# Kernel optimization log

Hardware: AMD Instinct MI355X
Metric: run time of the kernel (lower is better)

The kernel has to match this reference:

```python
import jax, jax.numpy as jnp
import numpy as np

N = 50000          # nodes
E = 800000         # edges (avg degree 16)
IN = 128           # input feature dim
HID = 64           # hidden dim per head
HEADS = 2          # attention heads (all but last layer)
OUT = 64           # out_dim (last layer, 1 head)
NC = 2             # num_classes
NEG_SLOPE = 0.2    # dgl GATConv leaky_relu slope


def setup_inputs() -> dict:
    key = jax.random.key(0)
    ks = jax.random.split(key, 20)
    rn = lambda k, shape, s=0.05: (jax.random.normal(k, shape, jnp.float32) * s)
    W_IO = HID * HEADS  # 128, width between GAT layers
    return {
        "x": rn(ks[0], (N, IN), 1.0),
        "src": jax.random.randint(ks[1], (E,), 0, N, dtype=jnp.int32),
        "dst": jax.random.randint(ks[2], (E,), 0, N, dtype=jnp.int32),
        # embedding_h: Linear(IN, HID*HEADS)
        "W_emb": rn(ks[3], (IN, W_IO)),
        "b_emb": jnp.zeros((W_IO,), jnp.float32),
        # GAT layer 0: in 128 -> 2 heads x 64
        "W0": rn(ks[4], (W_IO, HEADS * HID)),
        "al0": rn(ks[5], (HEADS, HID)),
        "ar0": rn(ks[6], (HEADS, HID)),
        "b0": jnp.zeros((HEADS * HID,), jnp.float32),
        # GAT layer 1: in 128 -> 2 heads x 64
        "W1": rn(ks[7], (W_IO, HEADS * HID)),
        "al1": rn(ks[8], (HEADS, HID)),
        "ar1": rn(ks[9], (HEADS, HID)),
        "b1": jnp.zeros((HEADS * HID,), jnp.float32),
        # GAT layer 2 (last): in 128 -> 1 head x OUT
        "W2": rn(ks[10], (W_IO, 1 * OUT)),
        "al2": rn(ks[11], (1, OUT)),
        "ar2": rn(ks[12], (1, OUT)),
        "b2": jnp.zeros((OUT,), jnp.float32),
        # edge scorer: Linear(2*OUT, NC)
        "Ws": rn(ks[13], (2 * OUT, NC)),
        "bs": jnp.zeros((NC,), jnp.float32),
    }


def gat_layer(h, src, dst, W, al, ar, b):
    """dgl GATConv + elu (GATLayer with batch_norm=False, residual=False)."""
    heads, out = al.shape
    feat = (h @ W).reshape(-1, heads, out)            # [N,H,D]
    el = jnp.sum(feat * al, axis=-1)                  # [N,H]
    er = jnp.sum(feat * ar, axis=-1)                  # [N,H]
    e = jax.nn.leaky_relu(el[src] + er[dst], NEG_SLOPE)  # [E,H]
    # edge softmax over incoming edges of each dst node
    emax = jax.ops.segment_max(e, dst, num_segments=N)   # [N,H]
    ex = jnp.exp(e - emax[dst])                          # [E,H]
    denom = jax.ops.segment_sum(ex, dst, num_segments=N) # [N,H]
    alpha = ex / jnp.where(denom[dst] > 0, denom[dst], 1.0)
    msg = feat[src] * alpha[:, :, None]                  # [E,H,D]
    rst = jax.ops.segment_sum(msg, dst, num_segments=N)  # [N,H,D]
    rst = rst.reshape(-1, heads * out) + b
    return jax.nn.elu(rst)


def reference(x, W_emb, b_emb, W0, al0, ar0, b0, W1, al1, ar1, b1,
              W2, al2, ar2, b2, Ws, bs, src, dst):
    h = x @ W_emb + b_emb                    # embedding_h (dropout p -> eval/identity)
    h = gat_layer(h, src, dst, W0, al0, ar0, b0)
    h = gat_layer(h, src, dst, W1, al1, ar1, b1)
    h = gat_layer(h, src, dst, W2, al2, ar2, b2)   # [N, OUT]
    # edge scorer on the scored subgraph: concat(src_h, dst_h) -> Linear
    he = jnp.concatenate([h[src], h[dst]], axis=1)  # [E, 2*OUT]
    return he @ Ws + bs                             # [E, NC]
```

## Files before the change

### kernel.cpp

```cpp
#include <hip/hip_runtime.h>
#include <hip/hip_bf16.h>
#include <math.h>


constexpr float SLOPE = 0.2f;

typedef __attribute__((ext_vector_type(8))) short bf16x8;
typedef __attribute__((ext_vector_type(4))) float f32x4;

__device__ __forceinline__ float b2f(unsigned short u) {
  union { unsigned int i; float f; } v;
  v.i = ((unsigned int)u) << 16;
  return v.f;
}
__device__ __forceinline__ unsigned short f2b(float f) {
  unsigned int x = __float_as_uint(f);
  unsigned int r = (x + 0x7fffu + ((x >> 16) & 1u)) >> 16;
  return (unsigned short)r;
}

__global__ void prep_wt_all(const float* __restrict__ Wa,
                            const float* __restrict__ Wb,
                            const float* __restrict__ Wc,
                            const float* __restrict__ Wd,
                            unsigned short* __restrict__ Ta,
                            unsigned short* __restrict__ Tb,
                            unsigned short* __restrict__ Tc,
                            unsigned short* __restrict__ Td) {
  int i = blockIdx.x * 256 + threadIdx.x;
  const float* W; unsigned short* T; int M; int off;
  if (i < 16384)      { W = Wa; T = Ta; M = 128; off = i; }
  else if (i < 32768) { W = Wb; T = Tb; M = 128; off = i - 16384; }
  else if (i < 49152) { W = Wc; T = Tc; M = 128; off = i - 32768; }
  else if (i < 57344) { W = Wd; T = Td; M = 64;  off = i - 49152; }
  else return;
  int k = off / M, m = off - k * M;
  T[m * 128 + k] = f2b(W[off]);
}

template<int M, bool AF32>
__global__ __launch_bounds__(256)
void gemm_mfma(const void* __restrict__ Xv,
               const unsigned short* __restrict__ Wt,
               const float* __restrict__ bias,
               const float* __restrict__ al, const float* __restrict__ ar,
               unsigned short* __restrict__ Yb,
               float* __restrict__ el, float* __restrict__ er, int N) {
  constexpr int NT = M / 16;
  constexpr int H = M / 64;

  const int tid = threadIdx.x;
  const int wave = tid >> 6;
  const int lane = tid & 63;
  const int r = lane & 15;
  const int kg = lane >> 4;
  const int rowbase = blockIdx.x * 64 + wave * 16;
  int grow = rowbase + r;
  int growc = grow < N ? grow : N - 1;

  f32x4 acc[NT];
  #pragma unroll
  for (int t = 0; t < NT; ++t) acc[t] = (f32x4){0.f, 0.f, 0.f, 0.f};

  #pragma unroll
  for (int kk = 0; kk < 4; ++kk) {
    const int k0 = kk * 32 + kg * 8;
    bf16x8 a;
    if constexpr (AF32) {
      const float* X = (const float*)Xv;
      const float4* xp =
          reinterpret_cast<const float4*>(X + (size_t)growc * 128 + k0);
      float4 x0 = xp[0], x1 = xp[1];
      a[0] = (short)f2b(x0.x); a[1] = (short)f2b(x0.y);
      a[2] = (short)f2b(x0.z); a[3] = (short)f2b(x0.w);
      a[4] = (short)f2b(x1.x); a[5] = (short)f2b(x1.y);
      a[6] = (short)f2b(x1.z); a[7] = (short)f2b(x1.w);
    } else {
      const unsigned short* Xb = (const unsigned short*)Xv;
      a = *reinterpret_cast<const bf16x8*>(Xb + (size_t)growc * 128 + k0);
    }
    #pragma unroll
    for (int t = 0; t < NT; ++t) {
      bf16x8 b = *reinterpret_cast<const bf16x8*>(
          Wt + (size_t)(t * 16 + r) * 128 + k0);
      acc[t] = __builtin_amdgcn_mfma_f32_16x16x32_bf16(a, b, acc[t], 0, 0, 0);
    }
  }

  float bv[NT];
  #pragma unroll
  for (int t = 0; t < NT; ++t) bv[t] = bias ? bias[t * 16 + r] : 0.f;
  float alv[NT], arv[NT];
  if (al != nullptr) {
    #pragma unroll
    for (int t = 0; t < NT; ++t) {
      alv[t] = al[t * 16 + r];
      arv[t] = ar[t * 16 + r];
    }
  }

  #pragma unroll
  for (int j = 0; j < 4; ++j) {
    int orow = rowbase + kg * 4 + j;
    bool ok = orow < N;
    if (ok) {
      #pragma unroll
      for (int t = 0; t < NT; ++t)
        Yb[(size_t)orow * M + t * 16 + r] = f2b(acc[t][j] + bv[t]);
    }
    if (al != nullptr) {
      float pl0 = 0.f, pr0 = 0.f, pl1 = 0.f, pr1 = 0.f;
      #pragma unroll
      for (int t = 0; t < 4; ++t) {
        pl0 += acc[t][j] * alv[t];
        pr0 += acc[t][j] * arv[t];
      }
      if constexpr (H == 2) {
        #pragma unroll
        for (int t = 4; t < 8; ++t) {
          pl1 += acc[t][j] * alv[t];
          pr1 += acc[t][j] * arv[t];
        }
      }
      #pragma unroll
      for (int off = 1; off < 16; off <<= 1) {
        pl0 += __shfl_xor(pl0, off);
        pr0 += __shfl_xor(pr0, off);
        if constexpr (H == 2) {
          pl1 += __shfl_xor(pl1, off);
          pr1 += __shfl_xor(pr1, off);
        }
      }
      if (r == 0 && ok) {
        if constexpr (H == 2) {
          el[orow * 2 + 0] = pl0; el[orow * 2 + 1] = pl1;
          er[orow * 2 + 0] = pr0; er[orow * 2 + 1] = pr1;
        } else {
          el[orow] = pl0;
          er[orow] = pr0;
        }
      }
    }
  }
}

__global__ __launch_bounds__(256)
void count_dst(const int* __restrict__ dst, int* __restrict__ cnt, int E) {
  int cls = blockIdx.x & 7;
  int grp = blockIdx.x >> 3;
  int nGrp = gridDim.x >> 3;
  for (int base = grp * 256; base < E; base += nGrp * 256) {
    int i = base + threadIdx.x;
    if (i < E) {
      int d = dst[i];
      if (((d >> 4) & 7) == cls) atomicAdd(&cnt[d], 1);
    }
  }
}

__global__ void scan1(const int* __restrict__ cnt, int* __restrict__ outv,
                      int* __restrict__ bsum, int n) {
  __shared__ int sm[256];
  int tid = threadIdx.x;
  int base = blockIdx.x * 1024 + tid * 4;
  int pre[4];
  int s = 0;
  #pragma unroll
  for (int j = 0; j < 4; ++j) {
    int idx = base + j;
    int v = (idx < n) ? ((cnt[idx] + 7) & ~7) : 0;
    pre[j] = s;
    s += v;
  }
  sm[tid] = s;
  __syncthreads();
  for (int off = 1; off < 256; off <<= 1) {
    int a = (tid >= off) ? sm[tid - off] : 0;
    __syncthreads();
    sm[tid] += a;
    __syncthreads();
  }
  int excl = sm[tid] - s;
  #pragma unroll
  for (int j = 0; j < 4; ++j) {
    int idx = base + j;
    if (idx < n) outv[idx] = excl + pre[j];
  }
  if (tid == 255) bsum[blockIdx.x] = sm[255];
}

__global__ void scan2(const int* __restrict__ bsum, int* __restrict__ btop,
                      int nb, int* __restrict__ row_last) {
  if (threadIdx.x == 0 && blockIdx.x == 0) {
    int s = 0;
    for (int i = 0; i < nb; ++i) { btop[i] = s; s += bsum[i]; }
    *row_last = s;
  }
}

__global__ void scan3(int* __restrict__ rp, int* __restrict__ cur,
                      const int* __restrict__ btop, int n) {
  int i = blockIdx.x * blockDim.x + threadIdx.x;
  if (i < n) {
    int v = rp[i] + btop[i >> 10];
    rp[i] = v;
    cur[i] = v;
  }
}

__global__ __launch_bounds__(256)
void scatter_edges(const int* __restrict__ src, const int* __restrict__ dst,
                   int* __restrict__ cur, int* __restrict__ s_csr, int E) {
  int cls = blockIdx.x & 7;
  int grp = blockIdx.x >> 3;
  int nGrp = gridDim.x >> 3;
  for (int base = grp * 256; base < E; base += nGrp * 256) {
    int i = base + threadIdx.x;
    if (i < E) {
      int d = dst[i];
      if (((d >> 4) & 7) == cls) {
        int p = atomicAdd(&cur[d], 1);
        s_csr[p] = src[i];
      }
    }
  }
}

template<int H>
__global__ __launch_bounds__(256)
void edge_prep(const int* __restrict__ s_csr, const float* __restrict__ el,
               const float* __restrict__ er, const int* __restrict__ rp,
               const int* __restrict__ ends, float2* __restrict__ edat,
               int N, int EP) {
  int tid = threadIdx.x;
  int node = blockIdx.x * 16 + (tid >> 4);
  int sl = tid & 15;
  if (node >= N) return;
  int beg = rp[node];
  int rend = ends[node];
  int pend = rp[node + 1];
  if constexpr (H == 2) {
    float2 re = reinterpret_cast<const float2*>(er)[node];
    for (int p = beg + sl; p < rend; p += 16) {
      int s = s_csr[p];
      float2 le = reinterpret_cast<const float2*>(el)[s];
      float e0 = le.x + re.x;
      float e1 = le.y + re.y;
      e0 = e0 > 0.f ? e0 : SLOPE * e0;
      e1 = e1 > 0.f ? e1 : SLOPE * e1;
      float sb = __int_as_float(s);
      edat[p] = make_float2(__expf(e0), sb);
      edat[(size_t)EP + p] = make_float2(__expf(e1), sb);
    }
    int p2 = rend + sl;
    if (p2 < pend) {
      edat[p2] = make_float2(0.f, __int_as_float(0));
      edat[(size_t)EP + p2] = make_float2(0.f, __int_as_float(0));
    }
  } else {
    float re = er[node];
    for (int p = beg + sl; p < rend; p += 16) {
      int s = s_csr[p];
      float ev = el[s] + re;
      ev = ev > 0.f ? ev : SLOPE * ev;
      edat[p] = make_float2(__expf(ev), __int_as_float(s));
    }
    int p2 = rend + sl;
    if (p2 < pend) edat[p2] = make_float2(0.f, __int_as_float(0));
  }
}

template<int H, bool SCORE>
__global__ __launch_bounds__(256)
void gat_aggregate(const unsigned short* __restrict__ featb,
                   const float2* __restrict__ edat,
                   const float* __restrict__ bias,
                   const int* __restrict__ row_ptr,
                   unsigned short* __restrict__ houtb,
                   const float* __restrict__ Wsc,
                   float* __restrict__ ps, float* __restrict__ pd,
                   int N, int EP) {
  int tid = threadIdx.x;
  int pid = blockIdx.x * 16 + (tid >> 4);
  int sl = tid & 15;
  const int NH = N * H;
  bool live = pid < NH;
  int pc = live ? pid : 0;
  int node, head;
  if constexpr (H == 2) { node = pc >> 1; head = pc & 1; }
  else                  { node = pc;      head = 0; }
  int beg = live ? row_ptr[node] : 0;
  int end = live ? row_ptr[node + 1] : 0;

  const int rowoff = head * 64 + sl * 4;
  const float2* edath = edat + (size_t)head * EP;

  float4 acc = make_float4(0.f, 0.f, 0.f, 0.f);
  float den = 0.f;

  for (int p = beg; p < end; p += 8) {
    #pragma unroll
    for (int j = 0; j < 8; ++j) {
      float2 ed = edath[p + j];
      float ex = ed.x;
      int s = __float_as_int(ed.y);
      ushort4 u = *reinterpret_cast<const ushort4*>(
          &featb[(size_t)s * (H * 64) + rowoff]);
      den += ex;
      acc.x += ex * b2f(u.x);
      acc.y += ex * b2f(u.y);
      acc.z += ex * b2f(u.z);
      acc.w += ex * b2f(u.w);
    }
  }

  if (live) {
    float inv = 1.f / (den > 0.f ? den : 1.f);
    float4 bv = reinterpret_cast<const float4*>(bias)[head * 16 + sl];
    float4 r;
    r.x = acc.x * inv + bv.x;
    r.y = acc.y * inv + bv.y;
    r.z = acc.z * inv + bv.z;
    r.w = acc.w * inv + bv.w;
    r.x = r.x > 0.f ? r.x : expm1f(r.x);
    r.y = r.y > 0.f ? r.y : expm1f(r.y);
    r.z = r.z > 0.f ? r.z : expm1f(r.z);
    r.w = r.w > 0.f ? r.w : expm1f(r.w);

    if constexpr (!SCORE) {
      ushort4 o;
      o.x = f2b(r.x); o.y = f2b(r.y); o.z = f2b(r.z); o.w = f2b(r.w);
      *reinterpret_cast<ushort4*>(&houtb[(size_t)pid * 64 + sl * 4]) = o;
    } else {
      float s0 = r.x * Wsc[(4 * sl + 0) * 2] + r.y * Wsc[(4 * sl + 1) * 2] +
                 r.z * Wsc[(4 * sl + 2) * 2] + r.w * Wsc[(4 * sl + 3) * 2];
      float s1 = r.x * Wsc[(4 * sl + 0) * 2 + 1] + r.y * Wsc[(4 * sl + 1) * 2 + 1] +
                 r.z * Wsc[(4 * sl + 2) * 2 + 1] + r.w * Wsc[(4 * sl + 3) * 2 + 1];
      float d0 = r.x * Wsc[(64 + 4 * sl + 0) * 2] + r.y * Wsc[(64 + 4 * sl + 1) * 2] +
                 r.z * Wsc[(64 + 4 * sl + 2) * 2] + r.w * Wsc[(64 + 4 * sl + 3) * 2];
      float d1 = r.x * Wsc[(64 + 4 * sl + 0) * 2 + 1] + r.y * Wsc[(64 + 4 * sl + 1) * 2 + 1] +
                 r.z * Wsc[(64 + 4 * sl + 2) * 2 + 1] + r.w * Wsc[(64 + 4 * sl + 3) * 2 + 1];
      #pragma unroll
      for (int off = 1; off < 16; off <<= 1) {
        s0 += __shfl_xor(s0, off);
        s1 += __shfl_xor(s1, off);
        d0 += __shfl_xor(d0, off);
        d1 += __shfl_xor(d1, off);
      }
      if (sl == 0) {
        ps[node * 2 + 0] = s0;
        ps[node * 2 + 1] = s1;
        pd[node * 2 + 0] = d0;
        pd[node * 2 + 1] = d1;
      }
    }
  }
}

__global__ void score_out(const int* __restrict__ src,
                          const int* __restrict__ dst,
                          const float* __restrict__ ps,
                          const float* __restrict__ pd,
                          const float* __restrict__ bs,
                          float* __restrict__ out, int E) {
  int i = blockIdx.x * blockDim.x + threadIdx.x;
  if (i < E) {
    int s = src[i], d = dst[i];
    float2 a = *reinterpret_cast<const float2*>(ps + (size_t)s * 2);
    float2 b = *reinterpret_cast<const float2*>(pd + (size_t)d * 2);
    float2 o;
    o.x = a.x + b.x + bs[0];
    o.y = a.y + b.y + bs[1];
    *reinterpret_cast<float2*>(out + (size_t)i * 2) = o;
  }
}

extern "C" void kernel_launch(void* const* d_in, const int* in_sizes, int n_in,
                              void* d_out, int out_size, void* d_ws,
                              size_t ws_size, hipStream_t stream) {
  const float* x    = (const float*)d_in[0];
  const int*   src  = (const int*)d_in[1];
  const int*   dst  = (const int*)d_in[2];
  const float* Wemb = (const float*)d_in[3];
  const float* bemb = (const float*)d_in[4];
  const float* W0   = (const float*)d_in[5];
  const float* al0  = (const float*)d_in[6];
  const float* ar0  = (const float*)d_in[7];
  const float* b0   = (const float*)d_in[8];
  const float* W1   = (const float*)d_in[9];
  const float* al1  = (const float*)d_in[10];
  const float* ar1  = (const float*)d_in[11];
  const float* b1   = (const float*)d_in[12];
  const float* W2   = (const float*)d_in[13];
  const float* al2  = (const float*)d_in[14];
  const float* ar2  = (const float*)d_in[15];
  const float* b2   = (const float*)d_in[16];
  const float* Wsc  = (const float*)d_in[17];
  const float* bsc  = (const float*)d_in[18];

  const int N = in_sizes[0] / 128;
  const int E = in_sizes[1];
  float* out = (float*)d_out;
  const int EP = E + 7 * N + 8;

  char* w = (char*)d_ws;
  float2* edat = (float2*)w; w += (size_t)EP * 2 * 8;
  unsigned short* Ab = (unsigned short*)w; w += (size_t)N * 128 * 2;
  unsigned short* Bb = (unsigned short*)w; w += (size_t)N * 128 * 2;
  unsigned short* WembT = (unsigned short*)w; w += 128 * 128 * 2;
  unsigned short* W0T   = (unsigned short*)w; w += 128 * 128 * 2;
  unsigned short* W1T   = (unsigned short*)w; w += 128 * 128 * 2;
  unsigned short* W2T   = (unsigned short*)w; w += 128 * 64 * 2;
  float* el  = (float*)w; w += (size_t)N * 2 * 4;
  float* er  = (float*)w; w += (size_t)N * 2 * 4;
  float* ps  = (float*)w; w += (size_t)N * 2 * 4;
  float* pd  = (float*)w; w += (size_t)N * 2 * 4;
  int* s_csr = (int*)w;   w += (size_t)EP * 4;
  int* cnt   = (int*)w;   w += (size_t)N * 4;
  int* rp    = (int*)w;   w += (size_t)(N + 4) * 4;
  int* cur   = (int*)w;   w += (size_t)N * 4;
  int* bsum  = (int*)w;   w += 4096;
  int* btop  = (int*)w;   w += 4096;

  prep_wt_all<<<(57344 + 255) / 256, 256, 0, stream>>>(
      Wemb, W0, W1, W2, WembT, W0T, W1T, W2T);

  hipMemsetAsync(cnt, 0, (size_t)N * 4, stream);
  count_dst<<<2048, 256, 0, stream>>>(dst, cnt, E);
  int nb = (N + 1023) / 1024;
  scan1<<<nb, 256, 0, stream>>>(cnt, rp, bsum, N);
  scan2<<<1, 64, 0, stream>>>(bsum, btop, nb, rp + N);
  scan3<<<(N + 255) / 256, 256, 0, stream>>>(rp, cur, btop, N);
  scatter_edges<<<2048, 256, 0, stream>>>(src, dst, cur, s_csr, E);

  const int gb = (N + 63) / 64;
  const int nbk = (N + 15) / 16;
  const int pb2 = (N * 2 + 15) / 16;
  const int pb1 = (N * 1 + 15) / 16;

  gemm_mfma<128, true><<<gb, 256, 0, stream>>>(x, WembT, bemb, nullptr,
                                               nullptr, Ab, nullptr, nullptr,
                                               N);

  gemm_mfma<128, false><<<gb, 256, 0, stream>>>(Ab, W0T, nullptr, al0, ar0,
                                                Bb, el, er, N);
  edge_prep<2><<<nbk, 256, 0, stream>>>(s_csr, el, er, rp, cur, edat, N, EP);
  gat_aggregate<2, false><<<pb2, 256, 0, stream>>>(Bb, edat, b0, rp, Ab,
                                                   nullptr, nullptr, nullptr,
                                                   N, EP);
  gemm_mfma<128, false><<<gb, 256, 0, stream>>>(Ab, W1T, nullptr, al1, ar1,
                                                Bb, el, er, N);
  edge_prep<2><<<nbk, 256, 0, stream>>>(s_csr, el, er, rp, cur, edat, N, EP);
  gat_aggregate<2, false><<<pb2, 256, 0, stream>>>(Bb, edat, b1, rp, Ab,
                                                   nullptr, nullptr, nullptr,
                                                   N, EP);
  gemm_mfma<64, false><<<gb, 256, 0, stream>>>(Ab, W2T, nullptr, al2, ar2,
                                               Bb, el, er, N);
  edge_prep<1><<<nbk, 256, 0, stream>>>(s_csr, el, er, rp, cur, edat, N, EP);
  gat_aggregate<1, true><<<pb1, 256, 0, stream>>>(Bb, edat, b2, rp, nullptr,
                                                  Wsc, ps, pd, N, EP);

  score_out<<<(E + 255) / 256, 256, 0, stream>>>(src, dst, ps, pd, bsc, out, E);
}
```

Baseline: 393.3 us.

## Sort nodes into degree bins to balance edge_prep and aggregate work per wave

Computes a per-node degree bucket (padded edge count divided by 8) during the scan, then builds an `order` permutation that groups nodes with equal bucket. edge_prep and gat_aggregate process nodes in that order, so the 16-lane groups sharing a wave walk similar edge counts and less time is lost to divergence. The cost is an extra atomic histogram in scan1, a wave-aggregated atomic placement in scan3, one indirection per node, and a loss of locality in row_ptr, feature writes and output writes, since the permutation scatters node IDs.

Result: slower. 795.1 us (+102.2%).

```diff
diff --git a/kernel.cpp b/kernel.cpp
--- a/kernel.cpp
+++ b/kernel.cpp
@@ -159,7 +159,8 @@
 }
 
 __global__ void scan1(const int* __restrict__ cnt, int* __restrict__ outv,
-                      int* __restrict__ bsum, int n) {
+                      int* __restrict__ bsum, int* __restrict__ binCnt,
+                      int n) {
   __shared__ int sm[256];
   int tid = threadIdx.x;
   int base = blockIdx.x * 1024 + tid * 4;
@@ -168,7 +169,12 @@
   #pragma unroll
   for (int j = 0; j < 4; ++j) {
     int idx = base + j;
-    int v = (idx < n) ? ((cnt[idx] + 7) & ~7) : 0;
+    int c = (idx < n) ? cnt[idx] : 0;
+    int v = (idx < n) ? ((c + 7) & ~7) : 0;
+    if (idx < n) {
+      int t = (c + 7) >> 3; if (t > 63) t = 63;
+      atomicAdd(&binCnt[t], 1);
+    }
     pre[j] = s;
     s += v;
   }
@@ -190,22 +196,52 @@
 }
 
 __global__ void scan2(const int* __restrict__ bsum, int* __restrict__ btop,
-                      int nb, int* __restrict__ row_last) {
+                      int nb, int* __restrict__ row_last,
+                      const int* __restrict__ binCnt,
+                      int* __restrict__ binCur) {
   if (threadIdx.x == 0 && blockIdx.x == 0) {
     int s = 0;
     for (int i = 0; i < nb; ++i) { btop[i] = s; s += bsum[i]; }
     *row_last = s;
+    int s2 = 0;
+    for (int i = 0; i < 64; ++i) { binCur[i] = s2; s2 += binCnt[i]; }
   }
 }
 
 __global__ void scan3(int* __restrict__ rp, int* __restrict__ cur,
-                      const int* __restrict__ btop, int n) {
+                      const int* __restrict__ btop,
+                      const int* __restrict__ cnt, int* __restrict__ binCur,
+                      int* __restrict__ order, int n) {
   int i = blockIdx.x * blockDim.x + threadIdx.x;
-  if (i < n) {
+  int lane = threadIdx.x & 63;
+  bool live = i < n;
+  int t = 0;
+  if (live) {
     int v = rp[i] + btop[i >> 10];
     rp[i] = v;
     cur[i] = v;
-  }
+    int c = cnt[i];
+    t = (c + 7) >> 3; if (t > 63) t = 63;
+  }
+  int pos = 0;
+  bool done = !live;
+  unsigned long long remaining = __ballot(!done);
+  while (remaining) {
+    int srcl = __ffsll((long long)remaining) - 1;
+    int tl = __shfl(t, srcl);
+    unsigned long long same = __ballot(!done && t == tl);
+    if (!done && t == tl) {
+      int lead = __ffsll((long long)same) - 1;
+      int cnt_ = __popcll(same);
+      int basep = 0;
+      if (lane == lead) basep = atomicAdd(&binCur[tl], cnt_);
+      basep = __shfl(basep, lead);
+      pos = basep + __popcll(same & ((1ull << lane) - 1ull));
+      done = true;
+    }
+    remaining &= ~same;
+  }
+  if (live) order[pos] = i;
 }
 
 __global__ __launch_bounds__(256)
@@ -230,12 +266,13 @@
 __global__ __launch_bounds__(256)
 void edge_prep(const int* __restrict__ s_csr, const float* __restrict__ el,
                const float* __restrict__ er, const int* __restrict__ rp,
-               const int* __restrict__ ends, float2* __restrict__ edat,
-               int N, int EP) {
+               const int* __restrict__ ends, const int* __restrict__ order,
+               float2* __restrict__ edat, int N, int EP) {
   int tid = threadIdx.x;
-  int node = blockIdx.x * 16 + (tid >> 4);
+  int g = blockIdx.x * 16 + (tid >> 4);
   int sl = tid & 15;
-  if (node >= N) return;
+  if (g >= N) return;
+  int node = order[g];
   int beg = rp[node];
   int rend = ends[node];
   int pend = rp[node + 1];
@@ -276,6 +313,7 @@
                    const float2* __restrict__ edat,
                    const float* __restrict__ bias,
                    const int* __restrict__ row_ptr,
+                   const int* __restrict__ order,
                    unsigned short* __restrict__ houtb,
                    const float* __restrict__ Wsc,
                    float* __restrict__ ps, float* __restrict__ pd,
@@ -287,8 +325,8 @@
   bool live = pid < NH;
   int pc = live ? pid : 0;
   int node, head;
-  if constexpr (H == 2) { node = pc >> 1; head = pc & 1; }
-  else                  { node = pc;      head = 0; }
+  if constexpr (H == 2) { node = order[pc >> 1]; head = pc & 1; }
+  else                  { node = order[pc];      head = 0; }
   int beg = live ? row_ptr[node] : 0;
   int end = live ? row_ptr[node + 1] : 0;
 
@@ -330,7 +368,8 @@
     if constexpr (!SCORE) {
       ushort4 o;
       o.x = f2b(r.x); o.y = f2b(r.y); o.z = f2b(r.z); o.w = f2b(r.w);
-      *reinterpret_cast<ushort4*>(&houtb[(size_t)pid * 64 + sl * 4]) = o;
+      *reinterpret_cast<ushort4*>(
+          &houtb[((size_t)node * H + head) * 64 + sl * 4]) = o;
     } else {
       float s0 = r.x * Wsc[(4 * sl + 0) * 2] + r.y * Wsc[(4 * sl + 1) * 2] +
                  r.z * Wsc[(4 * sl + 2) * 2] + r.w * Wsc[(4 * sl + 3) * 2];
@@ -417,20 +456,24 @@
   float* pd  = (float*)w; w += (size_t)N * 2 * 4;
   int* s_csr = (int*)w;   w += (size_t)EP * 4;
   int* cnt   = (int*)w;   w += (size_t)N * 4;
+  int* binCnt = (int*)w;  w += 64 * 4;
   int* rp    = (int*)w;   w += (size_t)(N + 4) * 4;
   int* cur   = (int*)w;   w += (size_t)N * 4;
+  int* order = (int*)w;   w += (size_t)N * 4;
+  int* binCur = (int*)w;  w += 64 * 4;
   int* bsum  = (int*)w;   w += 4096;
   int* btop  = (int*)w;   w += 4096;
 
   prep_wt_all<<<(57344 + 255) / 256, 256, 0, stream>>>(
       Wemb, W0, W1, W2, WembT, W0T, W1T, W2T);
 
-  hipMemsetAsync(cnt, 0, (size_t)N * 4, stream);
+  hipMemsetAsync(cnt, 0, (size_t)N * 4 + 64 * 4, stream);
   count_dst<<<2048, 256, 0, stream>>>(dst, cnt, E);
   int nb = (N + 1023) / 1024;
-  scan1<<<nb, 256, 0, stream>>>(cnt, rp, bsum, N);
-  scan2<<<1, 64, 0, stream>>>(bsum, btop, nb, rp + N);
-  scan3<<<(N + 255) / 256, 256, 0, stream>>>(rp, cur, btop, N);
+  scan1<<<nb, 256, 0, stream>>>(cnt, rp, bsum, binCnt, N);
+  scan2<<<1, 64, 0, stream>>>(bsum, btop, nb, rp + N, binCnt, binCur);
+  scan3<<<(N + 255) / 256, 256, 0, stream>>>(rp, cur, btop, cnt, binCur,
+                                             order, N);
   scatter_edges<<<2048, 256, 0, stream>>>(src, dst, cur, s_csr, E);
 
   const int gb = (N + 63) / 64;
@@ -444,21 +487,25 @@
 
   gemm_mfma<128, false><<<gb, 256, 0, stream>>>(Ab, W0T, nullptr, al0, ar0,
                                                 Bb, el, er, N);
-  edge_prep<2><<<nbk, 256, 0, stream>>>(s_csr, el, er, rp, cur, edat, N, EP);
-  gat_aggregate<2, false><<<pb2, 256, 0, stream>>>(Bb, edat, b0, rp, Ab,
-                                                   nullptr, nullptr, nullptr,
-                                                   N, EP);
+  edge_prep<2><<<nbk, 256, 0, stream>>>(s_csr, el, er, rp, cur, order, edat,
+                                        N, EP);
+  gat_aggregate<2, false><<<pb2, 256, 0, stream>>>(Bb, edat, b0, rp, order,
+                                                   Ab, nullptr, nullptr,
+                                                   nullptr, N, EP);
   gemm_mfma<128, false><<<gb, 256, 0, stream>>>(Ab, W1T, nullptr, al1, ar1,
                                                 Bb, el, er, N);
-  edge_prep<2><<<nbk, 256, 0, stream>>>(s_csr, el, er, rp, cur, edat, N, EP);
-  gat_aggregate<2, false><<<pb2, 256, 0, stream>>>(Bb, edat, b1, rp, Ab,
-                                                   nullptr, nullptr, nullptr,
-                                                   N, EP);
+  edge_prep<2><<<nbk, 256, 0, stream>>>(s_csr, el, er, rp, cur, order, edat,
+                                        N, EP);
+  gat_aggregate<2, false><<<pb2, 256, 0, stream>>>(Bb, edat, b1, rp, order,
+                                                   Ab, nullptr, nullptr,
+                                                   nullptr, N, EP);
   gemm_mfma<64, false><<<gb, 256, 0, stream>>>(Ab, W2T, nullptr, al2, ar2,
                                                Bb, el, er, N);
-  edge_prep<1><<<nbk, 256, 0, stream>>>(s_csr, el, er, rp, cur, edat, N, EP);
-  gat_aggregate<1, true><<<pb1, 256, 0, stream>>>(Bb, edat, b2, rp, nullptr,
-                                                  Wsc, ps, pd, N, EP);
+  edge_prep<1><<<nbk, 256, 0, stream>>>(s_csr, el, er, rp, cur, order, edat,
+                                        N, EP);
+  gat_aggregate<1, true><<<pb1, 256, 0, stream>>>(Bb, edat, b2, rp, order,
+                                                  nullptr, Wsc, ps, pd,
+                                                  N, EP);
 
   score_out<<<(E + 255) / 256, 256, 0, stream>>>(src, dst, ps, pd, bsc, out, E);
 }
```
